# Kernel tuning notes

Measured on AMD Instinct MI355X. Metric: run time of the kernel, lower is better.

## Reference

```python
import jax, jax.numpy as jnp
import numpy as np

B, T, N = 8, 12, 256
T_IN = S_IN = P_IN = 32
O_IN = 64
HID = 64
OUT = 64
HEADS = 4


def setup_inputs() -> dict:
    key = jax.random.key(0)
    ks = jax.random.split(key, 26)
    f = lambda k, shape: jax.random.normal(k, shape, jnp.float32) * 0.05
    return {
        'x': jax.random.normal(ks[0], (B, T, N, O_IN), jnp.float32),
        'adj': jax.random.randint(ks[1], (B, T, N, N), 0, 2, jnp.int32),
        'te': jax.random.normal(ks[2], (B, T, T_IN), jnp.float32),
        'se': jax.random.normal(ks[3], (N, S_IN), jnp.float32),
        'pe': jax.random.normal(ks[4], (N, P_IN), jnp.float32),
        # SPGAT linear layers
        'Wt': f(ks[5], (T_IN, HID)), 'bt': f(ks[6], (HID,)),
        'Ws': f(ks[7], (S_IN, HID)), 'bs': f(ks[8], (HID,)),
        'Wp': f(ks[9], (P_IN, HID)), 'bp': f(ks[10], (HID,)),
        'Wfc': f(ks[11], (HID, OUT)), 'bfc': f(ks[12], (OUT,)),
        'Wout': f(ks[13], (2 * OUT, OUT)), 'bout': f(ks[14], (OUT,)),
        # GAT layer 1 (heads=HEADS, concat)
        'W1': f(ks[15], (O_IN, HEADS * HID)), 'b1': f(ks[16], (HEADS * HID,)),
        'a1_src': f(ks[17], (HEADS, HID)), 'a1_dst': f(ks[18], (HEADS, HID)),
        # GAT layer 2 (heads=1)
        'W2': f(ks[19], (HEADS * HID, OUT)), 'b2': f(ks[20], (OUT,)),
        'a2_src': f(ks[21], (1, OUT)), 'a2_dst': f(ks[22], (1, OUT)),
    }


def _gat_conv(h, mask, W, b, a_src, a_dst, heads):
    # h: [B,T,N,Fin]; mask: [B,T,N,N] bool, mask[...,i,j] => edge i->j (coo row=src, col=dst)
    d = W.shape[1] // heads
    hp = (h @ W).reshape(h.shape[0], h.shape[1], h.shape[2], heads, d)  # [B,T,N,H,d]
    es = jnp.einsum('btnhd,hd->bthn', hp, a_src)  # source attention logits
    ed = jnp.einsum('btnhd,hd->bthn', hp, a_dst)  # target attention logits
    # scores[...,h,i,j] = leaky(es_i + ed_j), softmax over sources i per target j
    sc = jax.nn.leaky_relu(es[..., :, None] + ed[..., None, :], 0.2)  # [B,T,H,N,N]
    sc = jnp.where(mask[:, :, None, :, :], sc, jnp.float32(-1e9))
    alpha = jax.nn.softmax(sc, axis=-2)
    out = jnp.einsum('bthij,btihd->btjhd', alpha, hp)  # aggregate at target j
    return out.reshape(h.shape[0], h.shape[1], h.shape[2], heads * d) + b


def reference(x, adj, te, se, pe, Wt, bt, Ws, bs, Wp, bp, Wfc, bfc, Wout, bout,
              W1, b1, a1_src, a1_dst, W2, b2, a2_src, a2_dst):
    mask = adj != 0
    t = (te @ Wt + bt) @ Wfc + bfc          # [B,T,OUT]
    s = (se @ Ws + bs) @ Wfc + bfc          # [N,OUT]
    p = (pe @ Wp + bp) @ Wfc + bfc          # [N,OUT]
    sp = jnp.concatenate([s, p], axis=-1) @ Wout + bout  # [N,OUT]
    st = sp[None, None, :, :] + t[:, :, None, :]         # [B,T,N,OUT]
    h = jax.nn.elu(_gat_conv(x, mask, W1, b1, a1_src, a1_dst, HEADS))
    od = _gat_conv(h, mask, W2, b2, a2_src, a2_dst, 1)   # [B,T,N,OUT]
    return jnp.concatenate([od, st], axis=-1) @ Wout + bout
```

## Files before the change

kernel.cpp:

```cpp
#include <hip/hip_runtime.h>
#include <hip/hip_bf16.h>
#include <cstdint>

#define NNODE 256
#define NBT   96
#define LOG2E 1.4426950408889634f

typedef __attribute__((ext_vector_type(8))) short short8;
typedef __attribute__((ext_vector_type(4))) float f32x4;

__device__ __forceinline__ unsigned pack_bf16x2(float a, float b) {
  unsigned ua = __float_as_uint(a);
  unsigned ub = __float_as_uint(b);
  unsigned ra = (ua + 0x7FFFu + ((ua >> 16) & 1u)) >> 16;
  unsigned rb = ((ub + 0x7FFFu + ((ub >> 16) & 1u)) >> 16) << 16;
  return ra | rb;
}
__device__ __forceinline__ unsigned short bf16_rn(float a) {
  unsigned ua = __float_as_uint(a);
  return (unsigned short)((ua + 0x7FFFu + ((ua >> 16) & 1u)) >> 16);
}

__global__ __launch_bounds__(256) void setup_kernel(
    const int* __restrict__ adj, unsigned* __restrict__ mb,
    const float* __restrict__ te, const float* __restrict__ se, const float* __restrict__ pe,
    const float* __restrict__ Wt, const float* __restrict__ bt_,
    const float* __restrict__ Ws, const float* __restrict__ bs_,
    const float* __restrict__ Wp, const float* __restrict__ bp_,
    const float* __restrict__ Wfc, const float* __restrict__ bfc,
    const float* __restrict__ Wout, const float* __restrict__ bout,
    const float* __restrict__ W1, const float* __restrict__ W2,
    float* __restrict__ tW, float* __restrict__ spW,
    unsigned short* __restrict__ WoT, unsigned short* __restrict__ W1T,
    unsigned short* __restrict__ W2T) {
  const int blk = blockIdx.x, tid = threadIdx.x;
  __shared__ float A[64], Bv[64], C[64], D[64];

  if (blk < 768) {
    const int bt = blk >> 3, w = blk & 7, j = tid;
    const int* a = adj + (size_t)bt * NNODE * NNODE + (size_t)w * 32 * NNODE;
    unsigned v = 0;
#pragma unroll
    for (int b = 0; b < 32; ++b)
      v |= (a[b * NNODE + j] != 0 ? 1u : 0u) << b;
    mb[((size_t)bt * 8 + w) * 256 + j] = v;
  } else if (blk < 864) {
    const int row = blk - 768, j = tid & 63;
    if (tid < 64) {
      float h = bt_[j];
      for (int k = 0; k < 32; ++k) h += te[row * 32 + k] * Wt[k * 64 + j];
      A[j] = h;
    }
    __syncthreads();
    if (tid < 64) {
      float tv = bfc[j];
      for (int k = 0; k < 64; ++k) tv += A[k] * Wfc[k * 64 + j];
      Bv[j] = tv;
    }
    __syncthreads();
    if (tid < 64) {
      float tw = bout[j];
      for (int d = 0; d < 64; ++d) tw += Bv[d] * Wout[(64 + d) * 64 + j];
      tW[row * 64 + j] = tw;
    }
  } else if (blk < 1120) {
    const int n = blk - 864, j = tid & 63;
    float spv = 0.f;
    if (tid < 64) {
      float sh = bs_[j], ph = bp_[j];
      for (int k = 0; k < 32; ++k) {
        sh += se[n * 32 + k] * Ws[k * 64 + j];
        ph += pe[n * 32 + k] * Wp[k * 64 + j];
      }
      A[j] = sh; Bv[j] = ph;
    }
    __syncthreads();
    if (tid < 64) {
      float sv = bfc[j], pv = bfc[j];
      for (int k = 0; k < 64; ++k) {
        sv += A[k] * Wfc[k * 64 + j];
        pv += Bv[k] * Wfc[k * 64 + j];
      }
      C[j] = sv; D[j] = pv;
    }
    __syncthreads();
    if (tid < 64) {
      spv = bout[j];
      for (int k = 0; k < 64; ++k)
        spv += C[k] * Wout[k * 64 + j] + D[k] * Wout[(64 + k) * 64 + j];
    }
    __syncthreads();
    if (tid < 64) A[j] = spv;
    __syncthreads();
    if (tid < 64) {
      float spw = 0.f;
      for (int d = 0; d < 64; ++d) spw += A[d] * Wout[(64 + d) * 64 + j];
      spW[n * 64 + j] = spw;
    }
  } else if (blk == 1120) {
    {
      const int c = tid >> 2, d0 = (tid & 3) * 16;
#pragma unroll
      for (int i = 0; i < 16; ++i)
        WoT[c * 64 + d0 + i] = bf16_rn(Wout[(size_t)(d0 + i) * 64 + c]);
    }
    const int k = tid;
#pragma unroll
    for (int d = 0; d < 64; ++d)
      W2T[d * 256 + k] = bf16_rn(W2[(size_t)k * 64 + d]);
  } else {
    const int hd = tid;
    unsigned u[32];
#pragma unroll
    for (int p = 0; p < 32; ++p) {
      float a = W1[(size_t)(2 * p) * 256 + hd];
      float b = W1[(size_t)(2 * p + 1) * 256 + hd];
      u[p] = pack_bf16x2(a, b);
    }
    unsigned* o = (unsigned*)(W1T + (size_t)hd * 64);
#pragma unroll
    for (int p = 0; p < 8; ++p) {
      uint4 v;
      v.x = u[4 * p + 0]; v.y = u[4 * p + 1];
      v.z = u[4 * p + 2]; v.w = u[4 * p + 3];
      *reinterpret_cast<uint4*>(o + 4 * p) = v;
    }
  }
}

__global__ __launch_bounds__(512, 2) void fused1_kernel(
    const float* __restrict__ x, const unsigned* __restrict__ W1Tu,
    const unsigned* __restrict__ mbg, const float* __restrict__ a1s,
    const float* __restrict__ a1d, const float* __restrict__ b1,
    unsigned* __restrict__ hgl) {
  const int bt = blockIdx.x, head = blockIdx.y, z = blockIdx.z, tid = threadIdx.x;
  __shared__ union U {
    unsigned xb[256][36];
    unsigned hpT[64][132];
    unsigned short ob[128][72];
  } sm;
  __shared__ unsigned w1t[64][36];
  __shared__ unsigned mbs[1024];
  __shared__ float ess[256], eds[128], asv[64], adv[64];

  if (tid < 256) {
    const float* xrow = x + ((size_t)bt * NNODE + tid) * 64;
    unsigned u[32];
#pragma unroll
    for (int p = 0; p < 16; ++p) {
      float4 v = reinterpret_cast<const float4*>(xrow)[p];
      u[2 * p] = pack_bf16x2(v.x, v.y);
      u[2 * p + 1] = pack_bf16x2(v.z, v.w);
    }
#pragma unroll
    for (int p = 0; p < 8; ++p) {
      uint4 v; v.x = u[4 * p]; v.y = u[4 * p + 1]; v.z = u[4 * p + 2]; v.w = u[4 * p + 3];
      *reinterpret_cast<uint4*>(&sm.xb[tid][4 * p]) = v;
    }
    const int w = tid >> 5, col = (tid & 31) * 4;
    *reinterpret_cast<uint4*>(&mbs[w * 128 + col]) =
        *reinterpret_cast<const uint4*>(&mbg[(size_t)bt * 2048 + w * 256 + z * 128 + col]);
  } else {
    const int tt = tid - 256;
#pragma unroll
    for (int c = 0; c < 2; ++c) {
      const int idx = tt * 2 + c;
      const int r = idx >> 3, c4 = (idx & 7) * 4;
      *reinterpret_cast<uint4*>(&w1t[r][c4]) =
          *reinterpret_cast<const uint4*>(&W1Tu[(size_t)(head * 64 + r) * 32 + c4]);
    }
    if (tt < 64) asv[tt] = a1s[head * 64 + tt];
    else if (tt < 128) adv[tt - 64] = a1d[head * 64 + (tt - 64)];
  }
  __syncthreads();

  const int lane = tid & 63, wv = tid >> 6;
  const int m = lane & 15, q = lane >> 4;
  const f32x4 z4 = {0.f, 0.f, 0.f, 0.f};

  f32x4 cf[4][2];
#pragma unroll
  for (int mt = 0; mt < 4; ++mt)
#pragma unroll
    for (int nt = 0; nt < 2; ++nt) cf[mt][nt] = z4;
#pragma unroll
  for (int kt = 0; kt < 2; ++kt) {
    short8 af[4], bf[2];
#pragma unroll
    for (int mt = 0; mt < 4; ++mt)
      af[mt] = *reinterpret_cast<const short8*>(&w1t[mt * 16 + m][kt * 16 + q * 4]);
#pragma unroll
    for (int nt = 0; nt < 2; ++nt)
      bf[nt] = *reinterpret_cast<const short8*>(&sm.xb[wv * 32 + nt * 16 + m][kt * 16 + q * 4]);
#pragma unroll
    for (int mt = 0; mt < 4; ++mt)
#pragma unroll
      for (int nt = 0; nt < 2; ++nt)
        cf[mt][nt] = __builtin_amdgcn_mfma_f32_16x16x32_bf16(af[mt], bf[nt], cf[mt][nt], 0, 0, 0);
  }
  __syncthreads();

  {
    float pes0 = 0.f, pes1 = 0.f, ped0 = 0.f, ped1 = 0.f;
#pragma unroll
    for (int mt = 0; mt < 4; ++mt)
#pragma unroll
      for (int reg = 0; reg < 4; ++reg) {
        const int d = mt * 16 + q * 4 + reg;
        const float a = asv[d], bdv = adv[d];
        pes0 += cf[mt][0][reg] * a;  ped0 += cf[mt][0][reg] * bdv;
        pes1 += cf[mt][1][reg] * a;  ped1 += cf[mt][1][reg] * bdv;
      }
    pes0 += __shfl_xor(pes0, 16, 64); pes0 += __shfl_xor(pes0, 32, 64);
    pes1 += __shfl_xor(pes1, 16, 64); pes1 += __shfl_xor(pes1, 32, 64);
    ped0 += __shfl_xor(ped0, 16, 64); ped0 += __shfl_xor(ped0, 32, 64);
    ped1 += __shfl_xor(ped1, 16, 64); ped1 += __shfl_xor(ped1, 32, 64);
    if (q == 0) {
      const int n0 = wv * 32 + m, n1 = wv * 32 + 16 + m;
      ess[n0] = pes0 * LOG2E;
      ess[n1] = pes1 * LOG2E;
      if ((n0 >> 7) == z) eds[n0 & 127] = ped0 * LOG2E;
      if ((n1 >> 7) == z) eds[n1 & 127] = ped1 * LOG2E;
    }
  }

  {
    unsigned short* hpT16 = reinterpret_cast<unsigned short*>(&sm.hpT[0][0]);
#pragma unroll
    for (int mt = 0; mt < 4; ++mt)
#pragma unroll
      for (int nt = 0; nt < 2; ++nt)
#pragma unroll
        for (int reg = 0; reg < 4; ++reg) {
          const int d = mt * 16 + q * 4 + reg;
          const int n = wv * 32 + nt * 16 + m;
          hpT16[d * 264 + n] = bf16_rn(cf[mt][nt][reg]);
        }
  }
  __syncthreads();

  f32x4 cacc[4], cden = z4;
#pragma unroll
  for (int nt = 0; nt < 4; ++nt) cacc[nt] = z4;
  const float edv = eds[wv * 16 + m];
  const short8 ones8 = {(short)0x3F80, (short)0x3F80, (short)0x3F80, (short)0x3F80,
                        (short)0x3F80, (short)0x3F80, (short)0x3F80, (short)0x3F80};

  for (int kt = 0; kt < 8; ++kt) {
    short8 bfr[4];
#pragma unroll
    for (int nt = 0; nt < 4; ++nt)
      bfr[nt] = *reinterpret_cast<const short8*>(&sm.hpT[nt * 16 + m][kt * 16 + q * 4]);
    float e[8];
    *reinterpret_cast<float4*>(&e[0]) = *reinterpret_cast<const float4*>(&ess[kt * 32 + q * 8]);
    *reinterpret_cast<float4*>(&e[4]) = *reinterpret_cast<const float4*>(&ess[kt * 32 + q * 8 + 4]);
    const unsigned bits = mbs[kt * 128 + wv * 16 + m] >> (q * 8);
    float pv[8];
#pragma unroll
    for (int r = 0; r < 8; ++r) {
      float sc = e[r] + edv;
      sc = fmaxf(sc, 0.2f * sc);
      pv[r] = ((bits >> r) & 1u) ? exp2f(sc) : 0.f;
    }
    union { unsigned u[4]; short8 s; } A;
#pragma unroll
    for (int h = 0; h < 4; ++h) A.u[h] = pack_bf16x2(pv[2 * h], pv[2 * h + 1]);
#pragma unroll
    for (int nt = 0; nt < 4; ++nt)
      cacc[nt] = __builtin_amdgcn_mfma_f32_16x16x32_bf16(A.s, bfr[nt], cacc[nt], 0, 0, 0);
    cden = __builtin_amdgcn_mfma_f32_16x16x32_bf16(A.s, ones8, cden, 0, 0, 0);
  }
  __syncthreads();

  float b1v[4];
#pragma unroll
  for (int nt = 0; nt < 4; ++nt) b1v[nt] = b1[head * 64 + nt * 16 + m];
#pragma unroll
  for (int reg = 0; reg < 4; ++reg) {
    const int jl = wv * 16 + q * 4 + reg;
    const float inv = 1.f / fmaxf(cden[reg], 1e-30f);
#pragma unroll
    for (int nt = 0; nt < 4; ++nt) {
      float v = cacc[nt][reg] * inv + b1v[nt];
      v = v > 0.f ? v : expm1f(v);
      sm.ob[jl][nt * 16 + m] = bf16_rn(v);
    }
  }
  __syncthreads();

  unsigned* go = hgl + (size_t)bt * 32768 + (size_t)z * 128 * 128 + head * 32;
#pragma unroll
  for (int c = 0; c < 2; ++c) {
    const int idx = tid * 2 + c;
    const int jl = idx >> 3, c4 = (idx & 7) * 4;
    *reinterpret_cast<uint4*>(&go[(size_t)jl * 128 + c4]) =
        *reinterpret_cast<const uint4*>(&sm.ob[jl][c4 * 2]);
  }
}

__global__ __launch_bounds__(256, 2) void fused2_kernel(
    const unsigned* __restrict__ hglu, const unsigned* __restrict__ W2Tu,
    const unsigned* __restrict__ mbg, const float* __restrict__ a2s,
    const float* __restrict__ a2d, const float* __restrict__ b2,
    const unsigned* __restrict__ WoTu, const float* __restrict__ spW,
    const float* __restrict__ tW, float* __restrict__ out) {
  const int bt = blockIdx.x, jh = blockIdx.y, tid = threadIdx.x;
  const int jbase = jh * 64;
  __shared__ union U {
    struct { unsigned h_c[256][36]; unsigned w2t_c[64][36]; } fs;
    unsigned hpT[64][132];
    unsigned short ob[64][72];
  } sm;
  __shared__ unsigned wol[64][36];
  __shared__ unsigned mbs[512];
  __shared__ float ess[256], eds[64];
  __shared__ float a2sv[64], a2dv[64];

#pragma unroll
  for (int c = 0; c < 2; ++c) {
    int idx = tid * 2 + c;
    int row = idx >> 3, col = (idx & 7) * 4;
    *reinterpret_cast<uint4*>(&wol[row][col]) =
        *reinterpret_cast<const uint4*>(&WoTu[row * 32 + col]);
  }
  if (tid < 128) {
    int w = tid >> 4, col = (tid & 15) * 4;
    *reinterpret_cast<uint4*>(&mbs[w * 64 + col]) =
        *reinterpret_cast<const uint4*>(&mbg[(size_t)bt * 2048 + w * 256 + jbase + col]);
  } else if (tid < 192) {
    a2sv[tid - 128] = a2s[tid - 128];
  } else {
    a2dv[tid - 192] = a2d[tid - 192];
  }

  const int lane = tid & 63, wv = tid >> 6;
  const int m = lane & 15, q = lane >> 4;
  const f32x4 z4 = {0.f, 0.f, 0.f, 0.f};

  f32x4 cf[4][4];
#pragma unroll
  for (int mt = 0; mt < 4; ++mt)
#pragma unroll
    for (int nt = 0; nt < 4; ++nt) cf[mt][nt] = z4;

  for (int kc = 0; kc < 4; ++kc) {
    __syncthreads();
#pragma unroll
    for (int c = 0; c < 8; ++c) {
      int i4 = tid + c * 256;
      int n = i4 >> 3, col = (i4 & 7) * 4;
      *reinterpret_cast<uint4*>(&sm.fs.h_c[n][col]) =
          *reinterpret_cast<const uint4*>(&hglu[(size_t)bt * 32768 + n * 128 + kc * 32 + col]);
    }
#pragma unroll
    for (int c = 0; c < 2; ++c) {
      int idx = tid * 2 + c;
      int d = idx >> 3, col = (idx & 7) * 4;
      *reinterpret_cast<uint4*>(&sm.fs.w2t_c[d][col]) =
          *reinterpret_cast<const uint4*>(&W2Tu[d * 128 + kc * 32 + col]);
    }
    __syncthreads();
#pragma unroll
    for (int kt2 = 0; kt2 < 2; ++kt2) {
      short8 af[4], bf[4];
#pragma unroll
      for (int mt = 0; mt < 4; ++mt)
        af[mt] = *reinterpret_cast<const short8*>(&sm.fs.w2t_c[mt * 16 + m][kt2 * 16 + q * 4]);
#pragma unroll
      for (int nt = 0; nt < 4; ++nt)
        bf[nt] = *reinterpret_cast<const short8*>(&sm.fs.h_c[wv * 64 + nt * 16 + m][kt2 * 16 + q * 4]);
#pragma unroll
      for (int mt = 0; mt < 4; ++mt)
#pragma unroll
        for (int nt = 0; nt < 4; ++nt)
          cf[mt][nt] = __builtin_amdgcn_mfma_f32_16x16x32_bf16(af[mt], bf[nt], cf[mt][nt], 0, 0, 0);
    }
  }
  __syncthreads();

  {
    float pes[4] = {0.f, 0.f, 0.f, 0.f}, ped[4] = {0.f, 0.f, 0.f, 0.f};
#pragma unroll
    for (int mt = 0; mt < 4; ++mt)
#pragma unroll
      for (int reg = 0; reg < 4; ++reg) {
        const int d = mt * 16 + q * 4 + reg;
        const float a = a2sv[d], bdv = a2dv[d];
#pragma unroll
        for (int nt = 0; nt < 4; ++nt) {
          pes[nt] += cf[mt][nt][reg] * a;
          ped[nt] += cf[mt][nt][reg] * bdv;
        }
      }
#pragma unroll
    for (int nt = 0; nt < 4; ++nt) {
      pes[nt] += __shfl_xor(pes[nt], 16, 64); pes[nt] += __shfl_xor(pes[nt], 32, 64);
      ped[nt] += __shfl_xor(ped[nt], 16, 64); ped[nt] += __shfl_xor(ped[nt], 32, 64);
    }
    if (q == 0) {
#pragma unroll
      for (int nt = 0; nt < 4; ++nt) {
        const int n = wv * 64 + nt * 16 + m;
        ess[n] = pes[nt] * LOG2E;
        if (n >= jbase && n < jbase + 64) eds[n - jbase] = ped[nt] * LOG2E;
      }
    }
  }

  {
    unsigned short* hpT16 = reinterpret_cast<unsigned short*>(&sm.hpT[0][0]);
#pragma unroll
    for (int mt = 0; mt < 4; ++mt)
#pragma unroll
      for (int nt = 0; nt < 4; ++nt)
#pragma unroll
        for (int reg = 0; reg < 4; ++reg) {
          const int d = mt * 16 + q * 4 + reg;
          const int n = wv * 64 + nt * 16 + m;
          hpT16[d * 264 + n] = bf16_rn(cf[mt][nt][reg]);
        }
  }
  __syncthreads();

  f32x4 cacc[4], cden = z4;
#pragma unroll
  for (int nt = 0; nt < 4; ++nt) cacc[nt] = z4;
  const float edv = eds[wv * 16 + m];
  const short8 ones8 = {(short)0x3F80, (short)0x3F80, (short)0x3F80, (short)0x3F80,
                        (short)0x3F80, (short)0x3F80, (short)0x3F80, (short)0x3F80};

  for (int kt = 0; kt < 8; ++kt) {
    short8 bfr[4];
#pragma unroll
    for (int nt = 0; nt < 4; ++nt)
      bfr[nt] = *reinterpret_cast<const short8*>(&sm.hpT[nt * 16 + m][kt * 16 + q * 4]);
    float e[8];
    *reinterpret_cast<float4*>(&e[0]) = *reinterpret_cast<const float4*>(&ess[kt * 32 + q * 8]);
    *reinterpret_cast<float4*>(&e[4]) = *reinterpret_cast<const float4*>(&ess[kt * 32 + q * 8 + 4]);
    const unsigned bits = mbs[kt * 64 + wv * 16 + m] >> (q * 8);
    float pv[8];
#pragma unroll
    for (int r = 0; r < 8; ++r) {
      float sc = e[r] + edv;
      sc = fmaxf(sc, 0.2f * sc);
      pv[r] = ((bits >> r) & 1u) ? exp2f(sc) : 0.f;
    }
    union { unsigned u[4]; short8 s; } A;
#pragma unroll
    for (int h = 0; h < 4; ++h) A.u[h] = pack_bf16x2(pv[2 * h], pv[2 * h + 1]);
#pragma unroll
    for (int nt = 0; nt < 4; ++nt)
      cacc[nt] = __builtin_amdgcn_mfma_f32_16x16x32_bf16(A.s, bfr[nt], cacc[nt], 0, 0, 0);
    cden = __builtin_amdgcn_mfma_f32_16x16x32_bf16(A.s, ones8, cden, 0, 0, 0);
  }
  __syncthreads();

  float b2v[4];
#pragma unroll
  for (int nt = 0; nt < 4; ++nt) b2v[nt] = b2[nt * 16 + m];
#pragma unroll
  for (int reg = 0; reg < 4; ++reg) {
    const int jl = wv * 16 + q * 4 + reg;
    const float inv = 1.f / fmaxf(cden[reg], 1e-30f);
#pragma unroll
    for (int nt = 0; nt < 4; ++nt)
      sm.ob[jl][nt * 16 + m] = bf16_rn(cacc[nt][reg] * inv + b2v[nt]);
  }
  __syncthreads();

  f32x4 c2[4];
#pragma unroll
  for (int ct = 0; ct < 4; ++ct) c2[ct] = z4;
#pragma unroll
  for (int kt2 = 0; kt2 < 2; ++kt2) {
    short8 a2f = *reinterpret_cast<const short8*>(&sm.ob[wv * 16 + m][kt2 * 32 + q * 8]);
#pragma unroll
    for (int ct = 0; ct < 4; ++ct) {
      short8 bw = *reinterpret_cast<const short8*>(&wol[ct * 16 + m][kt2 * 16 + q * 4]);
      c2[ct] = __builtin_amdgcn_mfma_f32_16x16x32_bf16(a2f, bw, c2[ct], 0, 0, 0);
    }
  }
  float tWv[4];
#pragma unroll
  for (int ct = 0; ct < 4; ++ct) tWv[ct] = tW[bt * 64 + ct * 16 + m];
#pragma unroll
  for (int reg = 0; reg < 4; ++reg) {
    const int j = jbase + wv * 16 + q * 4 + reg;
#pragma unroll
    for (int ct = 0; ct < 4; ++ct) {
      const int cc = ct * 16 + m;
      out[((size_t)bt * NNODE + j) * 64 + cc] =
          c2[ct][reg] + spW[j * 64 + cc] + tWv[ct];
    }
  }
}

extern "C" void kernel_launch(void* const* d_in, const int* in_sizes, int n_in,
                              void* d_out, int out_size, void* d_ws, size_t ws_size,
                              hipStream_t stream) {
  const float* x    = (const float*)d_in[0];
  const int*   adj  = (const int*)d_in[1];
  const float* te   = (const float*)d_in[2];
  const float* se   = (const float*)d_in[3];
  const float* pe   = (const float*)d_in[4];
  const float* Wt   = (const float*)d_in[5];
  const float* bt_  = (const float*)d_in[6];
  const float* Ws   = (const float*)d_in[7];
  const float* bs_  = (const float*)d_in[8];
  const float* Wp   = (const float*)d_in[9];
  const float* bp_  = (const float*)d_in[10];
  const float* Wfc  = (const float*)d_in[11];
  const float* bfc  = (const float*)d_in[12];
  const float* Wout = (const float*)d_in[13];
  const float* bout = (const float*)d_in[14];
  const float* W1   = (const float*)d_in[15];
  const float* b1   = (const float*)d_in[16];
  const float* a1s  = (const float*)d_in[17];
  const float* a1d  = (const float*)d_in[18];
  const float* W2   = (const float*)d_in[19];
  const float* b2   = (const float*)d_in[20];
  const float* a2s  = (const float*)d_in[21];
  const float* a2d  = (const float*)d_in[22];

  char* ws = (char*)d_ws;
  unsigned*       mb   = (unsigned*)(ws);
  float*          tW   = (float*)(ws + 786432);
  float*          spW  = (float*)(ws + 811008);
  unsigned short* WoT  = (unsigned short*)(ws + 876544);
  unsigned short* W1T  = (unsigned short*)(ws + 884736);
  unsigned short* W2T  = (unsigned short*)(ws + 917504);
  unsigned*       hgl  = (unsigned*)(ws + 13533184);

  setup_kernel<<<1122, 256, 0, stream>>>(adj, mb, te, se, pe, Wt, bt_, Ws, bs_,
                                         Wp, bp_, Wfc, bfc, Wout, bout, W1, W2,
                                         tW, spW, WoT, W1T, W2T);
  fused1_kernel<<<dim3(NBT, 4, 2), 512, 0, stream>>>(x, (const unsigned*)W1T, mb,
                                                     a1s, a1d, b1, hgl);
  fused2_kernel<<<dim3(NBT, 4), 256, 0, stream>>>(hgl, (const unsigned*)W2T, mb,
                                                  a2s, a2d, b2, (const unsigned*)WoT,
                                                  spW, tW, (float*)d_out);
}
```

Baseline: 168.5 us.

## Merge fused1 target-half split so each block handles all 256 targets

Result: slower. 174.3 us (+3.4%).

```diff
diff --git a/kernel.cpp b/kernel.cpp
--- a/kernel.cpp
+++ b/kernel.cpp
@@ -133,15 +133,15 @@
     const unsigned* __restrict__ mbg, const float* __restrict__ a1s,
     const float* __restrict__ a1d, const float* __restrict__ b1,
     unsigned* __restrict__ hgl) {
-  const int bt = blockIdx.x, head = blockIdx.y, z = blockIdx.z, tid = threadIdx.x;
+  const int bt = blockIdx.x, head = blockIdx.y, tid = threadIdx.x;
   __shared__ union U {
     unsigned xb[256][36];
     unsigned hpT[64][132];
-    unsigned short ob[128][72];
+    unsigned short ob[256][72];
   } sm;
   __shared__ unsigned w1t[64][36];
-  __shared__ unsigned mbs[1024];
-  __shared__ float ess[256], eds[128], asv[64], adv[64];
+  __shared__ unsigned mbs[2048];
+  __shared__ float ess[256], eds[256], asv[64], adv[64];
 
   if (tid < 256) {
     const float* xrow = x + ((size_t)bt * NNODE + tid) * 64;
@@ -157,9 +157,6 @@
       uint4 v; v.x = u[4 * p]; v.y = u[4 * p + 1]; v.z = u[4 * p + 2]; v.w = u[4 * p + 3];
       *reinterpret_cast<uint4*>(&sm.xb[tid][4 * p]) = v;
     }
-    const int w = tid >> 5, col = (tid & 31) * 4;
-    *reinterpret_cast<uint4*>(&mbs[w * 128 + col]) =
-        *reinterpret_cast<const uint4*>(&mbg[(size_t)bt * 2048 + w * 256 + z * 128 + col]);
   } else {
     const int tt = tid - 256;
 #pragma unroll
@@ -172,6 +169,8 @@
     if (tt < 64) asv[tt] = a1s[head * 64 + tt];
     else if (tt < 128) adv[tt - 64] = a1d[head * 64 + (tt - 64)];
   }
+  *reinterpret_cast<uint4*>(&mbs[tid * 4]) =
+      *reinterpret_cast<const uint4*>(&mbg[(size_t)bt * 2048 + tid * 4]);
   __syncthreads();
 
   const int lane = tid & 63, wv = tid >> 6;
@@ -217,10 +216,8 @@
     ped1 += __shfl_xor(ped1, 16, 64); ped1 += __shfl_xor(ped1, 32, 64);
     if (q == 0) {
       const int n0 = wv * 32 + m, n1 = wv * 32 + 16 + m;
-      ess[n0] = pes0 * LOG2E;
-      ess[n1] = pes1 * LOG2E;
-      if ((n0 >> 7) == z) eds[n0 & 127] = ped0 * LOG2E;
-      if ((n1 >> 7) == z) eds[n1 & 127] = ped1 * LOG2E;
+      ess[n0] = pes0 * LOG2E;  eds[n0] = ped0 * LOG2E;
+      ess[n1] = pes1 * LOG2E;  eds[n1] = ped1 * LOG2E;
     }
   }
 
@@ -239,10 +236,16 @@
   }
   __syncthreads();
 
-  f32x4 cacc[4], cden = z4;
-#pragma unroll
-  for (int nt = 0; nt < 4; ++nt) cacc[nt] = z4;
-  const float edv = eds[wv * 16 + m];
+  f32x4 cacc[2][4], cden[2];
+#pragma unroll
+  for (int jt = 0; jt < 2; ++jt) {
+    cden[jt] = z4;
+#pragma unroll
+    for (int nt = 0; nt < 4; ++nt) cacc[jt][nt] = z4;
+  }
+  float edv[2];
+#pragma unroll
+  for (int jt = 0; jt < 2; ++jt) edv[jt] = eds[(wv * 2 + jt) * 16 + m];
   const short8 ones8 = {(short)0x3F80, (short)0x3F80, (short)0x3F80, (short)0x3F80,
                         (short)0x3F80, (short)0x3F80, (short)0x3F80, (short)0x3F80};
 
@@ -254,21 +257,25 @@
     float e[8];
     *reinterpret_cast<float4*>(&e[0]) = *reinterpret_cast<const float4*>(&ess[kt * 32 + q * 8]);
     *reinterpret_cast<float4*>(&e[4]) = *reinterpret_cast<const float4*>(&ess[kt * 32 + q * 8 + 4]);
-    const unsigned bits = mbs[kt * 128 + wv * 16 + m] >> (q * 8);
-    float pv[8];
-#pragma unroll
-    for (int r = 0; r < 8; ++r) {
-      float sc = e[r] + edv;
-      sc = fmaxf(sc, 0.2f * sc);
-      pv[r] = ((bits >> r) & 1u) ? exp2f(sc) : 0.f;
-    }
-    union { unsigned u[4]; short8 s; } A;
-#pragma unroll
-    for (int h = 0; h < 4; ++h) A.u[h] = pack_bf16x2(pv[2 * h], pv[2 * h + 1]);
-#pragma unroll
-    for (int nt = 0; nt < 4; ++nt)
-      cacc[nt] = __builtin_amdgcn_mfma_f32_16x16x32_bf16(A.s, bfr[nt], cacc[nt], 0, 0, 0);
-    cden = __builtin_amdgcn_mfma_f32_16x16x32_bf16(A.s, ones8, cden, 0, 0, 0);
+#pragma unroll
+    for (int jt = 0; jt < 2; ++jt) {
+      const int jr = (wv * 2 + jt) * 16 + m;
+      const unsigned bits = mbs[kt * 256 + jr] >> (q * 8);
+      float pv[8];
+#pragma unroll
+      for (int r = 0; r < 8; ++r) {
+        float sc = e[r] + edv[jt];
+        sc = fmaxf(sc, 0.2f * sc);
+        pv[r] = ((bits >> r) & 1u) ? exp2f(sc) : 0.f;
+      }
+      union { unsigned u[4]; short8 s; } A;
+#pragma unroll
+      for (int h = 0; h < 4; ++h) A.u[h] = pack_bf16x2(pv[2 * h], pv[2 * h + 1]);
+#pragma unroll
+      for (int nt = 0; nt < 4; ++nt)
+        cacc[jt][nt] = __builtin_amdgcn_mfma_f32_16x16x32_bf16(A.s, bfr[nt], cacc[jt][nt], 0, 0, 0);
+      cden[jt] = __builtin_amdgcn_mfma_f32_16x16x32_bf16(A.s, ones8, cden[jt], 0, 0, 0);
+    }
   }
   __syncthreads();
 
@@ -276,25 +283,28 @@
 #pragma unroll
   for (int nt = 0; nt < 4; ++nt) b1v[nt] = b1[head * 64 + nt * 16 + m];
 #pragma unroll
-  for (int reg = 0; reg < 4; ++reg) {
-    const int jl = wv * 16 + q * 4 + reg;
-    const float inv = 1.f / fmaxf(cden[reg], 1e-30f);
-#pragma unroll
-    for (int nt = 0; nt < 4; ++nt) {
-      float v = cacc[nt][reg] * inv + b1v[nt];
-      v = v > 0.f ? v : expm1f(v);
-      sm.ob[jl][nt * 16 + m] = bf16_rn(v);
-    }
-  }
-  __syncthreads();
-
-  unsigned* go = hgl + (size_t)bt * 32768 + (size_t)z * 128 * 128 + head * 32;
-#pragma unroll
-  for (int c = 0; c < 2; ++c) {
-    const int idx = tid * 2 + c;
-    const int jl = idx >> 3, c4 = (idx & 7) * 4;
-    *reinterpret_cast<uint4*>(&go[(size_t)jl * 128 + c4]) =
-        *reinterpret_cast<const uint4*>(&sm.ob[jl][c4 * 2]);
+  for (int jt = 0; jt < 2; ++jt) {
+#pragma unroll
+    for (int reg = 0; reg < 4; ++reg) {
+      const int j = (wv * 2 + jt) * 16 + q * 4 + reg;
+      const float inv = 1.f / fmaxf(cden[jt][reg], 1e-30f);
+#pragma unroll
+      for (int nt = 0; nt < 4; ++nt) {
+        float v = cacc[jt][nt][reg] * inv + b1v[nt];
+        v = v > 0.f ? v : expm1f(v);
+        sm.ob[j][nt * 16 + m] = bf16_rn(v);
+      }
+    }
+  }
+  __syncthreads();
+
+  unsigned* go = hgl + (size_t)bt * 32768 + head * 32;
+#pragma unroll
+  for (int c = 0; c < 4; ++c) {
+    const int idx = tid * 4 + c;
+    const int j = idx >> 3, c4 = (idx & 7) * 4;
+    *reinterpret_cast<uint4*>(&go[(size_t)j * 128 + c4]) =
+        *reinterpret_cast<const uint4*>(&sm.ob[j][c4 * 2]);
   }
 }
 
@@ -534,8 +544,8 @@
   setup_kernel<<<1122, 256, 0, stream>>>(adj, mb, te, se, pe, Wt, bt_, Ws, bs_,
                                          Wp, bp_, Wfc, bfc, Wout, bout, W1, W2,
                                          tW, spW, WoT, W1T, W2T);
-  fused1_kernel<<<dim3(NBT, 4, 2), 512, 0, stream>>>(x, (const unsigned*)W1T, mb,
-                                                     a1s, a1d, b1, hgl);
+  fused1_kernel<<<dim3(NBT, 4), 512, 0, stream>>>(x, (const unsigned*)W1T, mb,
+                                                  a1s, a1d, b1, hgl);
   fused2_kernel<<<dim3(NBT, 4), 256, 0, stream>>>(hgl, (const unsigned*)W2T, mb,
                                                   a2s, a2d, b2, (const unsigned*)WoT,
                                                   spW, tW, (float*)d_out);
```
